# Kernel optimization log

Hardware: AMD Instinct MI355X
Metric: run time of the kernel (lower is better)

## Reference

```python
import jax, jax.numpy as jnp
import numpy as np

D_MODEL = 1024
N_HEAD = 16
B, T = 4, 2048


def setup_inputs() -> dict:
    key = jax.random.key(0)
    k1, k2, k3, k4, k5 = jax.random.split(key, 5)
    s = 0.02
    return {
        "x": jax.random.normal(k1, (B, T, D_MODEL), dtype=jnp.float32),
        "w_attn": jax.random.normal(k2, (3 * D_MODEL, D_MODEL), dtype=jnp.float32) * s,
        "b_attn": jax.random.normal(k3, (3 * D_MODEL,), dtype=jnp.float32) * s,
        "w_proj": jax.random.normal(k4, (D_MODEL, D_MODEL), dtype=jnp.float32) * s,
        "b_proj": jax.random.normal(k5, (D_MODEL,), dtype=jnp.float32) * s,
    }


def reference(x, w_attn, b_attn, w_proj, b_proj):
    # x: [B, T, C]
    Bb, Tt, C = x.shape
    H = N_HEAD
    dk = C // H
    scale = 1.0 / np.sqrt(dk).astype(np.float32)

    qkv = x @ w_attn.T + b_attn                      # [B, T, 3C]
    q, k, v = jnp.split(qkv, 3, axis=-1)             # each [B, T, C]
    # -> [B, H, T, dk]
    q = q.reshape(Bb, Tt, H, dk).transpose(0, 2, 1, 3)
    k = k.reshape(Bb, Tt, H, dk).transpose(0, 2, 1, 3)
    v = v.reshape(Bb, Tt, H, dk).transpose(0, 2, 1, 3)

    att = jnp.einsum("bhqd,bhkd->bhqk", q, k) * scale   # [B, H, T, T]
    att = jax.nn.softmax(att, axis=-1)
    y = jnp.einsum("bhqk,bhkd->bhqd", att, v)            # [B, H, T, dk]
    y = y.transpose(0, 2, 1, 3).reshape(Bb, Tt, C)       # [B, T, C]
    return y @ w_proj.T + b_proj
```

## Files before the change

### kernel.cpp

```cpp
#include <hip/hip_runtime.h>
#include <hip/hip_bf16.h>

typedef __attribute__((ext_vector_type(8))) short short8;
typedef __attribute__((ext_vector_type(4))) short short4v;
typedef __attribute__((ext_vector_type(4))) float floatx4;
typedef __attribute__((ext_vector_type(16))) float floatx16;

#define B_ 4
#define T_ 2048
#define C_ 1024
#define H_ 16
#define DK_ 64
#define M_ (B_ * T_)
#define N3_ (3 * C_)

#define QSCALE 0.1803368801111243f

__device__ __forceinline__ unsigned short f2bf(float f) {
    union { float f; unsigned u; } v; v.f = f;
    unsigned r = v.u + 0x7fffu + ((v.u >> 16) & 1u);
    return (unsigned short)(r >> 16);
}
__device__ __forceinline__ unsigned fbits(float f) {
    union { float f; unsigned u; } v; v.f = f; return v.u;
}
__device__ __forceinline__ unsigned pack_bf16(float a, float b) {
#if __has_builtin(__builtin_amdgcn_cvt_pk_bf16_f32)
    typedef __attribute__((ext_vector_type(2))) __bf16 bf16x2;
    bf16x2 r = __builtin_amdgcn_cvt_pk_bf16_f32(a, b);
    union { bf16x2 v; unsigned u; } c; c.v = r; return c.u;
#else
    return __builtin_amdgcn_perm(fbits(b) + 0x8000u, fbits(a) + 0x8000u, 0x07060302u);
#endif
}

__device__ __forceinline__ void gload_lds16(const unsigned short* g, unsigned short* l) {
    __builtin_amdgcn_global_load_lds(
        (const __attribute__((address_space(1))) unsigned int*)(const void*)g,
        (__attribute__((address_space(3))) unsigned int*)(void*)l, 16, 0, 0);
}

#define NX4 (M_ * C_ / 4)
#define NA4 (N3_ * C_ / 4)
#define NP4 (C_ * C_ / 4)
__global__ __launch_bounds__(256) void cast3_kernel(const float* __restrict__ x,
                                                    const float* __restrict__ wa,
                                                    const float* __restrict__ wp,
                                                    unsigned short* __restrict__ xb,
                                                    unsigned short* __restrict__ wab,
                                                    unsigned short* __restrict__ wpb) {
    int i = blockIdx.x * 256 + threadIdx.x;
    const float* src; unsigned short* dst; int j;
    if (i < NX4) { src = x; dst = xb; j = i; }
    else if (i < NX4 + NA4) { src = wa; dst = wab; j = i - NX4; }
    else { src = wp; dst = wpb; j = i - NX4 - NA4; }
    float4 v = ((const float4*)src)[j];
    ushort4 o;
    o.x = f2bf(v.x); o.y = f2bf(v.y); o.z = f2bf(v.z); o.w = f2bf(v.w);
    ((ushort4*)dst)[j] = o;
}

#define BM 128
#define BN 128
#define BK 32

__global__ __launch_bounds__(256) void gemm_qkv(const unsigned short* __restrict__ A,
                                                const unsigned short* __restrict__ W,
                                                const float* __restrict__ bias,
                                                unsigned short* __restrict__ qout,
                                                unsigned short* __restrict__ kout,
                                                unsigned short* __restrict__ vout) {
    const int Kd = C_;
    __shared__ unsigned short As[BM * BK];
    __shared__ unsigned short Bs[BN * BK];
    int lin = blockIdx.y * gridDim.x + blockIdx.x;
    int cpx = (gridDim.x * gridDim.y) >> 3;
    int swz = (lin & 7) * cpx + (lin >> 3);
    int m0 = (swz / gridDim.x) * BM;
    int n0 = (swz % gridDim.x) * BN;
    int tid = threadIdx.x;
    int lane = tid & 63, w = tid >> 6;
    int wm = (w >> 1) * 64, wn = (w & 1) * 64;
    int l16 = lane & 15, quad = lane >> 4;
    int r4 = lane >> 2, c4 = (lane & 3) * 8;

    floatx4 acc[4][4] = {};
    for (int kt = 0; kt < Kd; kt += BK) {
        __syncthreads();
        for (int t = 0; t < 2; ++t) {
            int rbase = w * 32 + t * 16;
            gload_lds16(&A[(size_t)(m0 + rbase + r4) * Kd + kt + c4], &As[rbase * BK]);
            gload_lds16(&W[(size_t)(n0 + rbase + r4) * Kd + kt + c4], &Bs[rbase * BK]);
        }
        __syncthreads();
        short8 af[4], bf[4];
        for (int i = 0; i < 4; ++i)
            af[i] = *(const short8*)&As[(wm + 16 * i + l16) * BK + quad * 8];
        for (int j = 0; j < 4; ++j)
            bf[j] = *(const short8*)&Bs[(wn + 16 * j + l16) * BK + quad * 8];
        for (int i = 0; i < 4; ++i)
            for (int j = 0; j < 4; ++j)
                acc[i][j] = __builtin_amdgcn_mfma_f32_16x16x32_bf16(af[i], bf[j], acc[i][j], 0, 0, 0);
    }
    for (int i = 0; i < 4; ++i)
        for (int j = 0; j < 4; ++j) {
            int col = n0 + wn + 16 * j + l16;
            float bval = bias[col];
            int sec = col >> 10, cc = col & 1023;
            int h = cc >> 6, d = cc & 63;
            int m = m0 + wm + 16 * i + quad * 4;
            int b = m >> 11, t = m & (T_ - 1);
            int bh = b * H_ + h;
            if (sec == 2) {
                ushort4 o;
                o.x = f2bf(acc[i][j][0] + bval);
                o.y = f2bf(acc[i][j][1] + bval);
                o.z = f2bf(acc[i][j][2] + bval);
                o.w = f2bf(acc[i][j][3] + bval);
                *(ushort4*)&vout[((size_t)bh * DK_ + d) * T_ + t] = o;
            } else {
                float qs = (sec == 0) ? QSCALE : 1.0f;
                unsigned short* dst = (sec == 0) ? qout : kout;
                for (int r = 0; r < 4; ++r)
                    dst[((size_t)bh * T_ + t + r) * DK_ + d] = f2bf((acc[i][j][r] + bval) * qs);
            }
        }
}

__global__ __launch_bounds__(256) void gemm_proj(const unsigned short* __restrict__ A,
                                                 const unsigned short* __restrict__ W,
                                                 const float* __restrict__ bias,
                                                 float* __restrict__ out) {
    const int Kd = C_;
    __shared__ unsigned short As[BM * BK];
    __shared__ unsigned short Bs[BN * BK];
    int lin = blockIdx.y * gridDim.x + blockIdx.x;
    int cpx = (gridDim.x * gridDim.y) >> 3;
    int swz = (lin & 7) * cpx + (lin >> 3);
    int m0 = (swz / gridDim.x) * BM;
    int n0 = (swz % gridDim.x) * BN;
    int tid = threadIdx.x;
    int lane = tid & 63, w = tid >> 6;
    int wm = (w >> 1) * 64, wn = (w & 1) * 64;
    int l16 = lane & 15, quad = lane >> 4;
    int r4 = lane >> 2, c4 = (lane & 3) * 8;

    floatx4 acc[4][4] = {};
    for (int kt = 0; kt < Kd; kt += BK) {
        __syncthreads();
        for (int t = 0; t < 2; ++t) {
            int rbase = w * 32 + t * 16;
            gload_lds16(&A[(size_t)(m0 + rbase + r4) * Kd + kt + c4], &As[rbase * BK]);
            gload_lds16(&W[(size_t)(n0 + rbase + r4) * Kd + kt + c4], &Bs[rbase * BK]);
        }
        __syncthreads();
        short8 af[4], bf[4];
        for (int i = 0; i < 4; ++i)
            af[i] = *(const short8*)&As[(wm + 16 * i + l16) * BK + quad * 8];
        for (int j = 0; j < 4; ++j)
            bf[j] = *(const short8*)&Bs[(wn + 16 * j + l16) * BK + quad * 8];
        for (int i = 0; i < 4; ++i)
            for (int j = 0; j < 4; ++j)
                acc[i][j] = __builtin_amdgcn_mfma_f32_16x16x32_bf16(af[i], bf[j], acc[i][j], 0, 0, 0);
    }
    for (int i = 0; i < 4; ++i)
        for (int j = 0; j < 4; ++j) {
            int col = n0 + wn + 16 * j + l16;
            float bval = bias[col];
            for (int r = 0; r < 4; ++r) {
                int m = m0 + wm + 16 * i + quad * 4 + r;
                out[(size_t)m * C_ + col] = acc[i][j][r] + bval;
            }
        }
}

#define KT 64
#define LD 72

__global__ __launch_bounds__(256, 2) void attn_kernel(const unsigned short* __restrict__ Q,
                                                      const unsigned short* __restrict__ Kv,
                                                      const unsigned short* __restrict__ Vt,
                                                      unsigned short* __restrict__ Y) {
    __shared__ unsigned short smem[128 * LD];
    unsigned short* Ks = smem;
    unsigned short* Vts = smem + 64 * LD;

    int bid = blockIdx.x;
    int qt = bid >> 6;
    int bh = bid & 63;
    int b = bh >> 4, hh = bh & 15;
    const unsigned short* qh = Q + (size_t)bh * T_ * DK_;
    const unsigned short* kh = Kv + (size_t)bh * T_ * DK_;
    const unsigned short* vtg = Vt + (size_t)bh * DK_ * T_;

    int tid = threadIdx.x, lane = tid & 63, w = tid >> 6;
    int l31 = lane & 31, h = lane >> 5;
    int qrA = qt * 256 + w * 32;
    int qrB = qrA + 128;

    short8 qfA[4], qfB[4];
    for (int c = 0; c < 4; ++c) {
        qfA[c] = *(const short8*)&qh[(size_t)(qrA + l31) * DK_ + 16 * c + 8 * h];
        qfB[c] = *(const short8*)&qh[(size_t)(qrB + l31) * DK_ + 16 * c + 8 * h];
    }

    floatx16 oA0 = {}, oA1 = {}, oB0 = {}, oB1 = {};
    float lA = 0.f, lB = 0.f;

    for (int kt = 0; kt < T_; kt += KT) {
        __syncthreads();
        for (int it = 0; it < 2; ++it) {
            int idx = tid + it * 256;
            int r8 = idx >> 3, c8 = (idx & 7) * 8;
            *(short8*)&Ks[r8 * LD + c8] = *(const short8*)&kh[(size_t)(kt + r8) * DK_ + c8];
            int vd = r8 * LD + (c8 & 48) + ((c8 & 8) >> 1);
            union { short8 s; short4v q[2]; } u;
            u.s = *(const short8*)&vtg[(size_t)r8 * T_ + kt + c8];
            *(short4v*)&Vts[vd] = u.q[0];
            *(short4v*)&Vts[vd + 8] = u.q[1];
        }
        __syncthreads();

        floatx16 sA0 = {}, sA1 = {}, sB0 = {}, sB1 = {};
        for (int c = 0; c < 4; ++c) {
            short8 kf0 = *(const short8*)&Ks[l31 * LD + 16 * c + 8 * h];
            short8 kf1 = *(const short8*)&Ks[(32 + l31) * LD + 16 * c + 8 * h];
            sA0 = __builtin_amdgcn_mfma_f32_32x32x16_bf16(kf0, qfA[c], sA0, 0, 0, 0);
            sA1 = __builtin_amdgcn_mfma_f32_32x32x16_bf16(kf1, qfA[c], sA1, 0, 0, 0);
            sB0 = __builtin_amdgcn_mfma_f32_32x32x16_bf16(kf0, qfB[c], sB0, 0, 0, 0);
            sB1 = __builtin_amdgcn_mfma_f32_32x32x16_bf16(kf1, qfB[c], sB1, 0, 0, 0);
        }

        unsigned pA[16], pB[16];
        float tsA = 0.f, tsB = 0.f;
        for (int r2 = 0; r2 < 8; ++r2) {
            float a0 = __builtin_amdgcn_exp2f(sA0[2 * r2]);
            float a1 = __builtin_amdgcn_exp2f(sA0[2 * r2 + 1]);
            tsA += a0 + a1; pA[r2] = pack_bf16(a0, a1);
            float a2 = __builtin_amdgcn_exp2f(sA1[2 * r2]);
            float a3 = __builtin_amdgcn_exp2f(sA1[2 * r2 + 1]);
            tsA += a2 + a3; pA[8 + r2] = pack_bf16(a2, a3);
            float b0 = __builtin_amdgcn_exp2f(sB0[2 * r2]);
            float b1 = __builtin_amdgcn_exp2f(sB0[2 * r2 + 1]);
            tsB += b0 + b1; pB[r2] = pack_bf16(b0, b1);
            float b2 = __builtin_amdgcn_exp2f(sB1[2 * r2]);
            float b3 = __builtin_amdgcn_exp2f(sB1[2 * r2 + 1]);
            tsB += b2 + b3; pB[8 + r2] = pack_bf16(b2, b3);
        }
        lA += tsA; lB += tsB;

        for (int c = 0; c < 4; ++c) {
            short8 vf0 = *(const short8*)&Vts[l31 * LD + 16 * c + 8 * h];
            short8 vf1 = *(const short8*)&Vts[(32 + l31) * LD + 16 * c + 8 * h];
            union { unsigned u[4]; short8 s; } fA, fB;
            for (int j = 0; j < 4; ++j) { fA.u[j] = pA[4 * c + j]; fB.u[j] = pB[4 * c + j]; }
            oA0 = __builtin_amdgcn_mfma_f32_32x32x16_bf16(vf0, fA.s, oA0, 0, 0, 0);
            oA1 = __builtin_amdgcn_mfma_f32_32x32x16_bf16(vf1, fA.s, oA1, 0, 0, 0);
            oB0 = __builtin_amdgcn_mfma_f32_32x32x16_bf16(vf0, fB.s, oB0, 0, 0, 0);
            oB1 = __builtin_amdgcn_mfma_f32_32x32x16_bf16(vf1, fB.s, oB1, 0, 0, 0);
        }
    }

    float invA = 1.0f / (lA + __shfl_xor(lA, 32, 64));
    float invB = 1.0f / (lB + __shfl_xor(lB, 32, 64));
    int q_l = tid >> 1, seg = tid & 1;

    __syncthreads();
    for (int a = 0; a < 4; ++a) {
        ushort4 u;
        u.x = f2bf(oA0[4 * a + 0] * invA); u.y = f2bf(oA0[4 * a + 1] * invA);
        u.z = f2bf(oA0[4 * a + 2] * invA); u.w = f2bf(oA0[4 * a + 3] * invA);
        *(ushort4*)&smem[(w * 32 + l31) * LD + 8 * a + 4 * h] = u;
        ushort4 v;
        v.x = f2bf(oA1[4 * a + 0] * invA); v.y = f2bf(oA1[4 * a + 1] * invA);
        v.z = f2bf(oA1[4 * a + 2] * invA); v.w = f2bf(oA1[4 * a + 3] * invA);
        *(ushort4*)&smem[(w * 32 + l31) * LD + 32 + 8 * a + 4 * h] = v;
    }
    __syncthreads();
    {
        const unsigned short* srcp = &smem[(size_t)q_l * LD + seg * 32];
        unsigned short* dstp = &Y[((size_t)b * T_ + qt * 256 + q_l) * C_ + hh * DK_ + seg * 32];
        for (int j = 0; j < 4; ++j)
            *(short8*)&dstp[8 * j] = *(const short8*)&srcp[8 * j];
    }
    __syncthreads();
    for (int a = 0; a < 4; ++a) {
        ushort4 u;
        u.x = f2bf(oB0[4 * a + 0] * invB); u.y = f2bf(oB0[4 * a + 1] * invB);
        u.z = f2bf(oB0[4 * a + 2] * invB); u.w = f2bf(oB0[4 * a + 3] * invB);
        *(ushort4*)&smem[(w * 32 + l31) * LD + 8 * a + 4 * h] = u;
        ushort4 v;
        v.x = f2bf(oB1[4 * a + 0] * invB); v.y = f2bf(oB1[4 * a + 1] * invB);
        v.z = f2bf(oB1[4 * a + 2] * invB); v.w = f2bf(oB1[4 * a + 3] * invB);
        *(ushort4*)&smem[(w * 32 + l31) * LD + 32 + 8 * a + 4 * h] = v;
    }
    __syncthreads();
    {
        const unsigned short* srcp = &smem[(size_t)q_l * LD + seg * 32];
        unsigned short* dstp = &Y[((size_t)b * T_ + qt * 256 + 128 + q_l) * C_ + hh * DK_ + seg * 32];
        for (int j = 0; j < 4; ++j)
            *(short8*)&dstp[8 * j] = *(const short8*)&srcp[8 * j];
    }
}

extern "C" void kernel_launch(void* const* d_in, const int* in_sizes, int n_in,
                              void* d_out, int out_size, void* d_ws, size_t ws_size,
                              hipStream_t stream) {
    const float* x      = (const float*)d_in[0];
    const float* w_attn = (const float*)d_in[1];
    const float* b_attn = (const float*)d_in[2];
    const float* w_proj = (const float*)d_in[3];
    const float* b_proj = (const float*)d_in[4];
    float* out = (float*)d_out;

    unsigned short* ws = (unsigned short*)d_ws;
    unsigned short* xb  = ws;
    unsigned short* wab = xb  + (size_t)M_ * C_;
    unsigned short* wpb = wab + (size_t)N3_ * C_;
    unsigned short* qb  = wpb + (size_t)C_ * C_;
    unsigned short* kb  = qb  + (size_t)M_ * C_;
    unsigned short* vb  = kb  + (size_t)M_ * C_;
    unsigned short* yb  = vb  + (size_t)M_ * C_;

    cast3_kernel<<<(NX4 + NA4 + NP4) / 256, 256, 0, stream>>>(x, w_attn, w_proj, xb, wab, wpb);
    gemm_qkv<<<dim3(N3_ / BN, M_ / BM), 256, 0, stream>>>(xb, wab, b_attn, qb, kb, vb);
    attn_kernel<<<B_ * H_ * (T_ / 256), 256, 0, stream>>>(qb, kb, vb, yb);
    gemm_proj<<<dim3(C_ / BN, M_ / BM), 256, 0, stream>>>(yb, wpb, b_proj, out);
}
```

Measured before the change: 279.9 us.

## Double GEMM K-tile, XOR-swizzle LDS, stage Q/K epilogue through LDS

Both GEMMs now use a K-tile of 64 instead of 32, which halves the number of barrier-synchronised load/compute iterations. Global-to-LDS loads use an XOR swizzle on the 16-byte column chunk so that fragment reads avoid LDS bank conflicts. The QKV GEMM epilogue now branches once per block on its section; for Q and K it stages the bf16 tile in padded shared memory and writes 16-byte rows instead of scattered 2-byte stores. The cost is more shared memory per block and extra barriers in the epilogue, which may reduce occupancy.

```diff
diff --git a/kernel.cpp b/kernel.cpp
--- a/kernel.cpp
+++ b/kernel.cpp
@@ -62,7 +62,8 @@
 
 #define BM 128
 #define BN 128
-#define BK 32
+#define BK 64
+#define ELD 132
 
 __global__ __launch_bounds__(256) void gemm_qkv(const unsigned short* __restrict__ A,
                                                 const unsigned short* __restrict__ W,
@@ -70,7 +71,94 @@
                                                 unsigned short* __restrict__ qout,
                                                 unsigned short* __restrict__ kout,
                                                 unsigned short* __restrict__ vout) {
-    const int Kd = C_;
+    __shared__ unsigned short sh[BM * ELD];
+    unsigned short* As = sh;
+    unsigned short* Bs = sh + BM * BK;
+
+    int lin = blockIdx.y * gridDim.x + blockIdx.x;
+    int cpx = (gridDim.x * gridDim.y) >> 3;
+    int swz = (lin & 7) * cpx + (lin >> 3);
+    int m0 = (swz / gridDim.x) * BM;
+    int n0 = (swz % gridDim.x) * BN;
+    int tid = threadIdx.x;
+    int lane = tid & 63, w = tid >> 6;
+    int wm = (w >> 1) * 64, wn = (w & 1) * 64;
+    int l16 = lane & 15, quad = lane >> 4;
+    int srow = lane >> 3;
+    int scol = ((lane & 7) ^ srow) * 8;
+
+    floatx4 acc[4][4] = {};
+    for (int kt = 0; kt < C_; kt += BK) {
+        __syncthreads();
+        for (int t = 0; t < 4; ++t) {
+            int rbase = w * 32 + t * 8;
+            gload_lds16(&A[(size_t)(m0 + rbase + srow) * C_ + kt + scol], &As[rbase * BK]);
+            gload_lds16(&W[(size_t)(n0 + rbase + srow) * C_ + kt + scol], &Bs[rbase * BK]);
+        }
+        __syncthreads();
+#pragma unroll
+        for (int kc = 0; kc < 2; ++kc) {
+            int ch = ((kc * 4 + quad) ^ (l16 & 7)) * 8;
+            short8 af[4], bf[4];
+            for (int i = 0; i < 4; ++i)
+                af[i] = *(const short8*)&As[(wm + 16 * i + l16) * BK + ch];
+            for (int j = 0; j < 4; ++j)
+                bf[j] = *(const short8*)&Bs[(wn + 16 * j + l16) * BK + ch];
+            for (int i = 0; i < 4; ++i)
+                for (int j = 0; j < 4; ++j)
+                    acc[i][j] = __builtin_amdgcn_mfma_f32_16x16x32_bf16(af[i], bf[j], acc[i][j], 0, 0, 0);
+        }
+    }
+
+    int secb = n0 >> 10;
+    if (secb == 2) {
+        for (int i = 0; i < 4; ++i)
+            for (int j = 0; j < 4; ++j) {
+                int col = n0 + wn + 16 * j + l16;
+                float bval = bias[col];
+                int cc = col & 1023;
+                int h = cc >> 6, d = cc & 63;
+                int m = m0 + wm + 16 * i + quad * 4;
+                int b = m >> 11, t = m & (T_ - 1);
+                int bh = b * H_ + h;
+                ushort4 o;
+                o.x = f2bf(acc[i][j][0] + bval);
+                o.y = f2bf(acc[i][j][1] + bval);
+                o.z = f2bf(acc[i][j][2] + bval);
+                o.w = f2bf(acc[i][j][3] + bval);
+                *(ushort4*)&vout[((size_t)bh * DK_ + d) * T_ + t] = o;
+            }
+    } else {
+        float qs = (secb == 0) ? QSCALE : 1.0f;
+        unsigned short* dst = (secb == 0) ? qout : kout;
+        __syncthreads();
+        for (int i = 0; i < 4; ++i)
+            for (int j = 0; j < 4; ++j) {
+                int col = wn + 16 * j + l16;
+                float bval = bias[n0 + col];
+                for (int r = 0; r < 4; ++r) {
+                    int row = wm + 16 * i + quad * 4 + r;
+                    sh[row * ELD + col] = f2bf((acc[i][j][r] + bval) * qs);
+                }
+            }
+        __syncthreads();
+        for (int p = 0; p < 8; ++p) {
+            int row = p * 16 + (tid >> 4);
+            int cl = l16 * 8;
+            short8 v = *(const short8*)&sh[row * ELD + cl];
+            int cc = (n0 & 1023) + cl;
+            int h = cc >> 6, d = cc & 63;
+            int m = m0 + row, b = m >> 11, t = m & (T_ - 1);
+            int bh = b * H_ + h;
+            *(short8*)&dst[((size_t)bh * T_ + t) * DK_ + d] = v;
+        }
+    }
+}
+
+__global__ __launch_bounds__(256) void gemm_proj(const unsigned short* __restrict__ A,
+                                                 const unsigned short* __restrict__ W,
+                                                 const float* __restrict__ bias,
+                                                 float* __restrict__ out) {
     __shared__ unsigned short As[BM * BK];
     __shared__ unsigned short Bs[BN * BK];
     int lin = blockIdx.y * gridDim.x + blockIdx.x;
@@ -82,86 +170,30 @@
     int lane = tid & 63, w = tid >> 6;
     int wm = (w >> 1) * 64, wn = (w & 1) * 64;
     int l16 = lane & 15, quad = lane >> 4;
-    int r4 = lane >> 2, c4 = (lane & 3) * 8;
+    int srow = lane >> 3;
+    int scol = ((lane & 7) ^ srow) * 8;
 
     floatx4 acc[4][4] = {};
-    for (int kt = 0; kt < Kd; kt += BK) {
-        __syncthreads();
-        for (int t = 0; t < 2; ++t) {
-            int rbase = w * 32 + t * 16;
-            gload_lds16(&A[(size_t)(m0 + rbase + r4) * Kd + kt + c4], &As[rbase * BK]);
-            gload_lds16(&W[(size_t)(n0 + rbase + r4) * Kd + kt + c4], &Bs[rbase * BK]);
-        }
-        __syncthreads();
-        short8 af[4], bf[4];
-        for (int i = 0; i < 4; ++i)
-            af[i] = *(const short8*)&As[(wm + 16 * i + l16) * BK + quad * 8];
-        for (int j = 0; j < 4; ++j)
-            bf[j] = *(const short8*)&Bs[(wn + 16 * j + l16) * BK + quad * 8];
-        for (int i = 0; i < 4; ++i)
+    for (int kt = 0; kt < C_; kt += BK) {
+        __syncthreads();
+        for (int t = 0; t < 4; ++t) {
+            int rbase = w * 32 + t * 8;
+            gload_lds16(&A[(size_t)(m0 + rbase + srow) * C_ + kt + scol], &As[rbase * BK]);
+            gload_lds16(&W[(size_t)(n0 + rbase + srow) * C_ + kt + scol], &Bs[rbase * BK]);
+        }
+        __syncthreads();
+#pragma unroll
+        for (int kc = 0; kc < 2; ++kc) {
+            int ch = ((kc * 4 + quad) ^ (l16 & 7)) * 8;
+            short8 af[4], bf[4];
+            for (int i = 0; i < 4; ++i)
+                af[i] = *(const short8*)&As[(wm + 16 * i + l16) * BK + ch];
             for (int j = 0; j < 4; ++j)
-                acc[i][j] = __builtin_amdgcn_mfma_f32_16x16x32_bf16(af[i], bf[j], acc[i][j], 0, 0, 0);
-    }
-    for (int i = 0; i < 4; ++i)
-        for (int j = 0; j < 4; ++j) {
-            int col = n0 + wn + 16 * j + l16;
-            float bval = bias[col];
-            int sec = col >> 10, cc = col & 1023;
-            int h = cc >> 6, d = cc & 63;
-            int m = m0 + wm + 16 * i + quad * 4;
-            int b = m >> 11, t = m & (T_ - 1);
-            int bh = b * H_ + h;
-            if (sec == 2) {
-                ushort4 o;
-                o.x = f2bf(acc[i][j][0] + bval);
-                o.y = f2bf(acc[i][j][1] + bval);
-                o.z = f2bf(acc[i][j][2] + bval);
-                o.w = f2bf(acc[i][j][3] + bval);
-                *(ushort4*)&vout[((size_t)bh * DK_ + d) * T_ + t] = o;
-            } else {
-                float qs = (sec == 0) ? QSCALE : 1.0f;
-                unsigned short* dst = (sec == 0) ? qout : kout;
-                for (int r = 0; r < 4; ++r)
-                    dst[((size_t)bh * T_ + t + r) * DK_ + d] = f2bf((acc[i][j][r] + bval) * qs);
-            }
-        }
-}
-
-__global__ __launch_bounds__(256) void gemm_proj(const unsigned short* __restrict__ A,
-                                                 const unsigned short* __restrict__ W,
-                                                 const float* __restrict__ bias,
-                                                 float* __restrict__ out) {
-    const int Kd = C_;
-    __shared__ unsigned short As[BM * BK];
-    __shared__ unsigned short Bs[BN * BK];
-    int lin = blockIdx.y * gridDim.x + blockIdx.x;
-    int cpx = (gridDim.x * gridDim.y) >> 3;
-    int swz = (lin & 7) * cpx + (lin >> 3);
-    int m0 = (swz / gridDim.x) * BM;
-    int n0 = (swz % gridDim.x) * BN;
-    int tid = threadIdx.x;
-    int lane = tid & 63, w = tid >> 6;
-    int wm = (w >> 1) * 64, wn = (w & 1) * 64;
-    int l16 = lane & 15, quad = lane >> 4;
-    int r4 = lane >> 2, c4 = (lane & 3) * 8;
-
-    floatx4 acc[4][4] = {};
-    for (int kt = 0; kt < Kd; kt += BK) {
-        __syncthreads();
-        for (int t = 0; t < 2; ++t) {
-            int rbase = w * 32 + t * 16;
-            gload_lds16(&A[(size_t)(m0 + rbase + r4) * Kd + kt + c4], &As[rbase * BK]);
-            gload_lds16(&W[(size_t)(n0 + rbase + r4) * Kd + kt + c4], &Bs[rbase * BK]);
-        }
-        __syncthreads();
-        short8 af[4], bf[4];
-        for (int i = 0; i < 4; ++i)
-            af[i] = *(const short8*)&As[(wm + 16 * i + l16) * BK + quad * 8];
-        for (int j = 0; j < 4; ++j)
-            bf[j] = *(const short8*)&Bs[(wn + 16 * j + l16) * BK + quad * 8];
-        for (int i = 0; i < 4; ++i)
-            for (int j = 0; j < 4; ++j)
-                acc[i][j] = __builtin_amdgcn_mfma_f32_16x16x32_bf16(af[i], bf[j], acc[i][j], 0, 0, 0);
+                bf[j] = *(const short8*)&Bs[(wn + 16 * j + l16) * BK + ch];
+            for (int i = 0; i < 4; ++i)
+                for (int j = 0; j < 4; ++j)
+                    acc[i][j] = __builtin_amdgcn_mfma_f32_16x16x32_bf16(af[i], bf[j], acc[i][j], 0, 0, 0);
+        }
     }
     for (int i = 0; i < 4; ++i)
         for (int j = 0; j < 4; ++j) {
```

Result: faster. 262.3 us, median of 3 (-6.3%).
